# Kernel tuning notes

Hardware: AMD Instinct MI355X
Metric: run time of the kernel (lower is better)

The kernel has to match this reference:

```python
import jax, jax.numpy as jnp
import numpy as np

EPS = 1e-5
SLOPE = 0.01  # LeakyReLU default negative_slope
D_STATE = 16


def leaky(x):
    return jnp.where(x >= 0, x, SLOPE * x)


def instance_norm(x):
    # InstanceNorm3d(affine=False): normalize per (n, c) over spatial dims
    m = x.mean(axis=(2, 3, 4), keepdims=True)
    v = x.var(axis=(2, 3, 4), keepdims=True)
    return (x - m) * jax.lax.rsqrt(v + EPS)


def conv3d(x, w, b, groups=1, pad=0):
    y = jax.lax.conv_general_dilated(
        x, w, (1, 1, 1), [(pad, pad)] * 3,
        dimension_numbers=('NCDHW', 'OIDHW', 'NCDHW'),
        feature_group_count=groups)
    return y + b[None, :, None, None, None]


def conv_transpose2(x, w, b):
    # ConvTranspose3d(k=2, s=2): non-overlapping, so it is a pure einsum+interleave
    # x: [n,c,d,h,w], w: [c,o,2,2,2] (torch layout)
    y = jnp.einsum('ncdhw,coijk->nodihjwk', x, w)
    n, o, d, _, h, _, ww, _ = y.shape
    return y.reshape(n, o, 2 * d, 2 * h, 2 * ww) + b[None, :, None, None, None]


def selective_scan(u, dt, A, B, C, D):
    # u, dt: [b,l,d]; A: [d,n]; B, C: [b,l,n]; D: [d]
    dA = jnp.exp(dt[..., None] * A)                              # [b,l,d,n]
    dBu = dt[..., None] * B[:, :, None, :] * u[..., None]        # [b,l,d,n]

    def step(h, inp):
        dA_t, dBu_t, C_t = inp
        h = dA_t * h + dBu_t                                     # [b,d,n]
        y = jnp.einsum('bdn,bn->bd', h, C_t)
        return h, y

    h0 = jnp.zeros((u.shape[0],) + A.shape, u.dtype)
    _, ys = jax.lax.scan(
        step, h0,
        (dA.transpose(1, 0, 2, 3), dBu.transpose(1, 0, 2, 3), C.transpose(1, 0, 2)))
    return ys.transpose(1, 0, 2) + u * D                         # [b,l,d]


def mamba_block(x, in_proj_w, conv1d_w, conv1d_b, x_proj_w,
                dt_proj_w, dt_proj_b, A_log, D_param, out_proj_w):
    # x: [b,l,c]
    dt_rank = dt_proj_w.shape[1]
    xz = x @ in_proj_w.T                                         # [b,l,2*d_inner]
    xi, z = jnp.split(xz, 2, axis=-1)
    # causal depthwise conv1d over sequence (torch pads d_conv-1 both sides, keeps [:L])
    xi_c = xi.transpose(0, 2, 1)                                 # [b,d_inner,l]
    xi_c = jax.lax.conv_general_dilated(
        xi_c, conv1d_w, (1,), [(conv1d_w.shape[-1] - 1, 0)],
        dimension_numbers=('NCH', 'OIH', 'NCH'),
        feature_group_count=xi_c.shape[1])
    xi = jax.nn.silu(xi_c + conv1d_b[None, :, None]).transpose(0, 2, 1)  # [b,l,d_inner]
    x_dbl = xi @ x_proj_w.T
    dt, B, C = jnp.split(x_dbl, [dt_rank, dt_rank + D_STATE], axis=-1)
    dt = jax.nn.softplus(dt @ dt_proj_w.T + dt_proj_b)
    A = -jnp.exp(A_log)
    y = selective_scan(xi, dt, A, B, C, D_param)
    y = y * jax.nn.silu(z)
    return y @ out_proj_w.T


def layer_norm(x, w, b):
    m = x.mean(-1, keepdims=True)
    v = x.var(-1, keepdims=True)
    return (x - m) * jax.lax.rsqrt(v + EPS) * w + b


def up_forward(x1, x2, up_w, up_b, dc1_w, dc1_b, dc2_w, dc2_b, dc3_w, dc3_b,
               ln_w, ln_b, in_proj_w, conv1d_w, conv1d_b, x_proj_w,
               dt_proj_w, dt_proj_b, A_log, D_param, out_proj_w):
    x1 = conv_transpose2(x1, up_w, up_b)
    dZ = x2.shape[2] - x1.shape[2]
    dY = x2.shape[3] - x1.shape[3]
    dX = x2.shape[4] - x1.shape[4]
    x1 = jnp.pad(x1, ((0, 0), (0, 0),
                      (dZ // 2, dZ - dZ // 2),
                      (dY // 2, dY - dY // 2),
                      (dX // 2, dX - dX // 2)))
    x = jnp.concatenate([x2, x1], axis=1)
    # DoubleConv (residual=False since in_channels != out_channels)
    x = leaky(instance_norm(conv3d(x, dc1_w, dc1_b)))
    x = leaky(instance_norm(conv3d(x, dc2_w, dc2_b, groups=8, pad=1)))
    x = leaky(instance_norm(conv3d(x, dc3_w, dc3_b)))
    # MambaLayer over flattened spatial tokens
    b, c, d, h, w = x.shape
    t = x.transpose(0, 2, 3, 4, 1).reshape(b, d * h * w, c)
    t = layer_norm(t, ln_w, ln_b)
    t = mamba_block(t, in_proj_w, conv1d_w, conv1d_b, x_proj_w,
                    dt_proj_w, dt_proj_b, A_log, D_param, out_proj_w)
    return t.reshape(b, d, h, w, c).transpose(0, 4, 1, 2, 3)


def setup_inputs() -> dict:
    key = jax.random.key(0)
    ks = jax.random.split(key, 20)
    c_out = 32      # out_channels / d_model
    d_inner = 64    # expand * d_model
    dt_rank = 2     # ceil(32/16)
    s = 0.02
    return {
        'x1': jax.random.normal(ks[0], (2, 32, 8, 16, 16), jnp.float32),
        'x2': jax.random.normal(ks[1], (2, 32, 16, 32, 32), jnp.float32),
        'up_w': jax.random.normal(ks[2], (32, 32, 2, 2, 2), jnp.float32) * s,
        'up_b': jnp.zeros((32,), jnp.float32),
        'dc1_w': jax.random.normal(ks[3], (32, 64, 1, 1, 1), jnp.float32) * s,
        'dc1_b': jnp.zeros((32,), jnp.float32),
        'dc2_w': jax.random.normal(ks[4], (32, 4, 3, 3, 3), jnp.float32) * s,
        'dc2_b': jnp.zeros((32,), jnp.float32),
        'dc3_w': jax.random.normal(ks[5], (32, 32, 1, 1, 1), jnp.float32) * s,
        'dc3_b': jnp.zeros((32,), jnp.float32),
        'ln_w': jnp.ones((c_out,), jnp.float32),
        'ln_b': jnp.zeros((c_out,), jnp.float32),
        'in_proj_w': jax.random.normal(ks[6], (2 * d_inner, c_out), jnp.float32) * s,
        'conv1d_w': jax.random.normal(ks[7], (d_inner, 1, 4), jnp.float32) * s,
        'conv1d_b': jnp.zeros((d_inner,), jnp.float32),
        'x_proj_w': jax.random.normal(ks[8], (dt_rank + 2 * D_STATE, d_inner), jnp.float32) * s,
        'dt_proj_w': jax.random.normal(ks[9], (d_inner, dt_rank), jnp.float32) * s,
        'dt_proj_b': jnp.full((d_inner,), -4.0, jnp.float32),
        'A_log': jnp.log(jnp.tile(jnp.arange(1.0, D_STATE + 1.0, dtype=jnp.float32), (d_inner, 1))),
        'D_param': jnp.ones((d_inner,), jnp.float32),
        'out_proj_w': jax.random.normal(ks[10], (c_out, d_inner), jnp.float32) * s,
    }


def reference(x1, x2, up_w, up_b, dc1_w, dc1_b, dc2_w, dc2_b, dc3_w, dc3_b,
              ln_w, ln_b, in_proj_w, conv1d_w, conv1d_b, x_proj_w,
              dt_proj_w, dt_proj_b, A_log, D_param, out_proj_w):
    return up_forward(x1, x2, up_w, up_b, dc1_w, dc1_b, dc2_w, dc2_b, dc3_w, dc3_b,
                      ln_w, ln_b, in_proj_w, conv1d_w, conv1d_b, x_proj_w,
                      dt_proj_w, dt_proj_b, A_log, D_param, out_proj_w)
```

## Files before the change

kernel.cpp:

```cpp
#include <hip/hip_runtime.h>

#define TPB 256
#define S_TOT 16384
#define NCHUNK 256
#define EPS 1e-5f
#define SLOPE 0.01f

__device__ __forceinline__ float leakyf(float v){ return v > 0.f ? v : SLOPE * v; }
__device__ __forceinline__ float siluf(float v){ return v / (1.f + __expf(-v)); }

__global__ __launch_bounds__(TPB) void k_upc1(
    const float* __restrict__ x1, const float* __restrict__ x2,
    const float* __restrict__ upw, const float* __restrict__ upb,
    const float* __restrict__ w1, const float* __restrict__ b1,
    float* __restrict__ c1, float* st1p) {
  __shared__ float wq[8192];
  __shared__ float sup[64*33];
  __shared__ float red[4][8][2];
  int t = threadIdx.x, bid = blockIdx.x;
  int sb = bid & 255, n = bid >> 8;
  int p = t & 63, os = t >> 6;
  int s = sb*64 + p;
  for (int i = t; i < 8192; i += TPB) wq[i] = upw[i];
  __syncthreads();
  int z = s >> 10, y = (s >> 5) & 31, x = s & 31;
  int tap = ((z & 1)*2 + (y & 1))*2 + (x & 1);
  int xb = n*65536 + (z >> 1)*256 + (y >> 1)*16 + (x >> 1);
  float xv[32];
  #pragma unroll
  for (int c = 0; c < 32; c++) xv[c] = x1[xb + c*2048];
  float up[8];
  #pragma unroll
  for (int j = 0; j < 8; j++) up[j] = upb[os*8 + j];
  #pragma unroll
  for (int c = 0; c < 32; c++) {
    #pragma unroll
    for (int j = 0; j < 8; j++)
      up[j] += xv[c] * wq[c*256 + (os*8 + j)*8 + tap];
  }
  #pragma unroll
  for (int j = 0; j < 8; j++) sup[p*33 + os*8 + j] = up[j];
  __syncthreads();
  int c0 = os*8;
  float acc[8];
  #pragma unroll
  for (int j = 0; j < 8; j++) acc[j] = b1[c0 + j];
  const float* px2 = x2 + n*32*S_TOT + s;
  #pragma unroll
  for (int i = 0; i < 32; i++) {
    float v = px2[i*S_TOT];
    #pragma unroll
    for (int j = 0; j < 8; j++) acc[j] += v * w1[(c0 + j)*64 + i];
  }
  #pragma unroll
  for (int o = 0; o < 32; o++) {
    float v = sup[p*33 + o];
    #pragma unroll
    for (int j = 0; j < 8; j++) acc[j] += v * w1[(c0 + j)*64 + 32 + o];
  }
  #pragma unroll
  for (int j = 0; j < 8; j++)
    c1[(n*32 + c0 + j)*S_TOT + s] = acc[j];
  int wv = t >> 6;
  #pragma unroll
  for (int j = 0; j < 8; j++) {
    float sm = acc[j], sq = acc[j]*acc[j];
    #pragma unroll
    for (int o = 32; o > 0; o >>= 1) { sm += __shfl_down(sm, o); sq += __shfl_down(sq, o); }
    if ((t & 63) == 0) { red[wv][j][0] = sm; red[wv][j][1] = sq; }
  }
  __syncthreads();
  if (t < 64) {
    int w2 = t >> 4, j = (t >> 1) & 7, m = t & 1;
    st1p[((n*32 + w2*8 + j)*2 + m)*256 + sb] = red[w2][j][m];
  }
}

__global__ __launch_bounds__(TPB) void k_conv2(
    const float* __restrict__ c1, const float* __restrict__ w,
    const float* __restrict__ bias, const float* st1p,
    float* __restrict__ c2, float* st2p) {
  __shared__ float ws[432];
  __shared__ float smom[4][2];
  __shared__ float mrs[4][2];
  __shared__ float red[4][4][2];
  int bid = blockIdx.x, t = threadIdx.x;
  int sb = bid & 63, g = (bid >> 6) & 7, n = bid >> 9;
  int s = (sb << 8) + t;
  for (int i = t; i < 432; i += TPB) ws[i] = w[(g*4)*108 + i];
  {
    int pp = t >> 5, l = t & 31;
    if (pp < 8) {
      int j = pp & 3, m = pp >> 2;
      const float* sp = st1p + ((n*32 + g*4 + j)*2 + m)*256;
      float v = 0.f;
      #pragma unroll
      for (int k = 0; k < 8; k++) v += sp[l + 32*k];
      v += __shfl_down(v, 16); v += __shfl_down(v, 8); v += __shfl_down(v, 4);
      v += __shfl_down(v, 2);  v += __shfl_down(v, 1);
      if (l == 0) smom[j][m] = v;
    }
  }
  __syncthreads();
  if (t < 4) {
    float m = smom[t][0] * (1.f/S_TOT);
    mrs[t][0] = m; mrs[t][1] = rsqrtf(smom[t][1]*(1.f/S_TOT) - m*m + EPS);
  }
  __syncthreads();
  int z = s >> 10, y = (s >> 5) & 31, x = s & 31;
  float mx0 = (x > 0) ? 1.f : 0.f, mx2 = (x < 31) ? 1.f : 0.f;
  float acc[4];
  #pragma unroll
  for (int oc = 0; oc < 4; oc++) acc[oc] = bias[g*4 + oc];
  const float* pbase = c1 + (n*32 + g*4)*S_TOT;
  #pragma unroll
  for (int ic = 0; ic < 4; ic++) {
    const float* pc = pbase + ic*S_TOT;
    float m = mrs[ic][0], rs = mrs[ic][1];
    #pragma unroll
    for (int dz = 0; dz < 3; dz++) {
      int zz = z + dz - 1;
      int zc = zz < 0 ? 0 : (zz > 15 ? 15 : zz);
      float vz = (zz >= 0 && zz < 16) ? 1.f : 0.f;
      #pragma unroll
      for (int dy = 0; dy < 3; dy++) {
        int yy = y + dy - 1;
        int yc = yy < 0 ? 0 : (yy > 31 ? 31 : yy);
        float vzy = vz * ((yy >= 0 && yy < 32) ? 1.f : 0.f);
        const float* pr = pc + zc*1024 + yc*32 + x;
        float p0 = leakyf((pr[-1] - m)*rs) * (vzy*mx0);
        float p1 = leakyf((pr[ 0] - m)*rs) * vzy;
        float p2 = leakyf((pr[ 1] - m)*rs) * (vzy*mx2);
        int wb = ic*27 + dz*9 + dy*3;
        #pragma unroll
        for (int oc = 0; oc < 4; oc++) {
          const float* wo = &ws[oc*108 + wb];
          acc[oc] += p0*wo[0] + p1*wo[1] + p2*wo[2];
        }
      }
    }
  }
  float sm[4], sq[4];
  #pragma unroll
  for (int oc = 0; oc < 4; oc++) {
    c2[(n*32 + g*4 + oc)*S_TOT + s] = acc[oc];
    sm[oc] = acc[oc]; sq[oc] = acc[oc]*acc[oc];
  }
  #pragma unroll
  for (int o = 32; o > 0; o >>= 1) {
    #pragma unroll
    for (int oc = 0; oc < 4; oc++) {
      sm[oc] += __shfl_down(sm[oc], o);
      sq[oc] += __shfl_down(sq[oc], o);
    }
  }
  int lane = t & 63, wv = t >> 6;
  if (lane == 0) {
    #pragma unroll
    for (int oc = 0; oc < 4; oc++) { red[wv][oc][0] = sm[oc]; red[wv][oc][1] = sq[oc]; }
  }
  __syncthreads();
  if (t < 8) {
    int oc = t & 3, m = t >> 2;
    float a = red[0][oc][m] + red[1][oc][m] + red[2][oc][m] + red[3][oc][m];
    st2p[((n*32 + g*4 + oc)*2 + m)*64 + sb] = a;
  }
}

__global__ __launch_bounds__(TPB) void k_conv3(
    const float* __restrict__ c2, const float* __restrict__ w,
    const float* __restrict__ bias, const float* st2p,
    float* __restrict__ c3, float* st3p) {
  __shared__ float ws[256];
  __shared__ float ssum[32][2];
  __shared__ float mrs[32][2];
  __shared__ float red[4][8][2];
  int t = threadIdx.x;
  int idx = blockIdx.x * TPB + t;
  int s = idx & 16383;
  int n = (idx >> 14) & 1;
  int q = idx >> 15;
  int sb = blockIdx.x & 63;
  int c0 = q*8;
  if (t < 256) ws[t] = w[c0*32 + t];
  if (t < 64) {
    int c = t >> 1, m = t & 1;
    const float* sp = st2p + ((n*32 + c)*2 + m)*64;
    float v = 0.f;
    #pragma unroll
    for (int k = 0; k < 64; k++) v += sp[k];
    ssum[c][m] = v;
  }
  __syncthreads();
  if (t < 32) {
    float m = ssum[t][0] * (1.f/S_TOT);
    mrs[t][0] = m; mrs[t][1] = rsqrtf(ssum[t][1]*(1.f/S_TOT) - m*m + EPS);
  }
  __syncthreads();
  const float* pin = c2 + n*32*S_TOT + s;
  float acc[8];
  #pragma unroll
  for (int j = 0; j < 8; j++) acc[j] = bias[c0 + j];
  #pragma unroll
  for (int i = 0; i < 32; i++) {
    float v = leakyf((pin[i*S_TOT] - mrs[i][0]) * mrs[i][1]);
    #pragma unroll
    for (int j = 0; j < 8; j++) acc[j] += v * ws[j*32 + i];
  }
  #pragma unroll
  for (int j = 0; j < 8; j++)
    c3[(n*32 + c0 + j)*S_TOT + s] = acc[j];
  int wv = t >> 6;
  #pragma unroll
  for (int j = 0; j < 8; j++) {
    float sm = acc[j], sq = acc[j]*acc[j];
    #pragma unroll
    for (int o = 32; o > 0; o >>= 1) { sm += __shfl_down(sm, o); sq += __shfl_down(sq, o); }
    if ((t & 63) == 0) { red[wv][j][0] = sm; red[wv][j][1] = sq; }
  }
  __syncthreads();
  if (t < 16) {
    int j = t >> 1, m = t & 1;
    float a = red[0][j][m] + red[1][j][m] + red[2][j][m] + red[3][j][m];
    st3p[((n*32 + c0 + j)*2 + m)*64 + sb] = a;
  }
}

__global__ __launch_bounds__(TPB) void k_token(
    const float* __restrict__ c3, const float* st3p,
    const float* __restrict__ lnw, const float* __restrict__ lnb,
    const float* __restrict__ ipw, const float* __restrict__ c1w,
    const float* __restrict__ c1b, const float* __restrict__ xpw,
    const float* __restrict__ dtw, const float* __restrict__ dtbi,
    float* __restrict__ zb, float* __restrict__ u, float* __restrict__ dt,
    float* __restrict__ Bb, float* __restrict__ Cc) {
  __shared__ float W2T[4096];
  __shared__ float xpT[2176];
  __shared__ float tk[19*33];
  __shared__ float sxi[19*64];
  __shared__ float su2[16*65];
  __shared__ float xd[16*34];
  __shared__ float S1[128], S2[128];
  __shared__ float mv[19][2];
  __shared__ float mrs[32][2];
  __shared__ float ssum[32][2];
  int t = threadIdx.x, bid = blockIdx.x;
  int tok0 = bid * 16;
  int n = tok0 >> 14, s0 = tok0 & 16383;
  if (t < 64) {
    int c = t >> 1, m = t & 1;
    const float* sp = st3p + ((n*32 + c)*2 + m)*64;
    float v = 0.f;
    #pragma unroll
    for (int k = 0; k < 64; k++) v += sp[k];
    ssum[c][m] = v;
  }
  for (int i = t; i < 4096; i += TPB) {
    int f = i >> 5, c = i & 31;
    W2T[c*128 + f] = ipw[i] * lnw[c];
  }
  for (int i = t; i < 2176; i += TPB) {
    int f = i >> 6, dd = i & 63;
    xpT[dd*34 + f] = xpw[i];
  }
  __syncthreads();
  if (t < 32) {
    float m = ssum[t][0] * (1.f/S_TOT);
    mrs[t][0] = m; mrs[t][1] = rsqrtf(ssum[t][1]*(1.f/S_TOT) - m*m + EPS);
  }
  if (t < 128) {
    float a = 0.f, b2 = 0.f;
    #pragma unroll
    for (int c = 0; c < 32; c++) { a += W2T[c*128 + t]; b2 += ipw[t*32 + c]*lnb[c]; }
    S1[t] = a; S2[t] = b2;
  }
  __syncthreads();
  for (int i = t; i < 608; i += TPB) {
    int lt = i >> 5, c = i & 31;
    int sg = s0 - 3 + lt;
    int sgc = sg < 0 ? 0 : sg;
    float raw = c3[(n*32 + c)*S_TOT + sgc];
    tk[lt*33 + c] = leakyf((raw - mrs[c][0]) * mrs[c][1]);
  }
  __syncthreads();
  if (t < 19) {
    float mean = 0.f;
    #pragma unroll
    for (int c = 0; c < 32; c++) mean += tk[t*33 + c];
    mean *= (1.f/32.f);
    float var = 0.f;
    #pragma unroll
    for (int c = 0; c < 32; c++) { float d2 = tk[t*33 + c] - mean; var += d2*d2; }
    mv[t][0] = mean; mv[t][1] = rsqrtf(var*(1.f/32.f) + EPS);
  }
  __syncthreads();
  for (int i = t; i < 19*128; i += TPB) {
    int lt = i >> 7, f = i & 127;
    float acc = 0.f;
    #pragma unroll
    for (int c = 0; c < 32; c++) acc += W2T[c*128 + f] * tk[lt*33 + c];
    float r = mv[lt][1]*(acc - mv[lt][0]*S1[f]) + S2[f];
    int sg = s0 - 3 + lt;
    if (f < 64) {
      sxi[lt*64 + f] = (sg < 0) ? 0.f : r;
    } else if (lt >= 3) {
      zb[(tok0 + lt - 3)*64 + (f - 64)] = r;
    }
  }
  __syncthreads();
  int ch = t & 63;
  float cw0 = c1w[ch*4], cw1 = c1w[ch*4+1], cw2 = c1w[ch*4+2], cw3 = c1w[ch*4+3];
  float cb = c1b[ch];
  #pragma unroll
  for (int r = 0; r < 4; r++) {
    int lt = (t >> 6) + 4*r;
    float acc = cb + sxi[lt*64 + ch]*cw0 + sxi[(lt+1)*64 + ch]*cw1
                   + sxi[(lt+2)*64 + ch]*cw2 + sxi[(lt+3)*64 + ch]*cw3;
    float uv = siluf(acc);
    u[(tok0 + lt)*64 + ch] = uv;
    su2[lt*65 + ch] = uv;
  }
  __syncthreads();
  for (int i = t; i < 544; i += TPB) {
    int lt = i / 34, f = i - lt*34;
    float a = 0.f;
    #pragma unroll
    for (int dd = 0; dd < 64; dd++) a += xpT[dd*34 + f] * su2[lt*65 + dd];
    xd[lt*34 + f] = a;
  }
  __syncthreads();
  float dw0 = dtw[ch*2], dw1 = dtw[ch*2+1], db = dtbi[ch];
  #pragma unroll
  for (int r = 0; r < 4; r++) {
    int lt = (t >> 6) + 4*r;
    int token = tok0 + lt;
    float dv = xd[lt*34]*dw0 + xd[lt*34 + 1]*dw1 + db;
    dt[token*64 + ch] = fmaxf(dv, 0.f) + log1pf(__expf(-fabsf(dv)));
    if (ch < 16)      Bb[token*16 + ch]      = xd[lt*34 + 2 + ch];
    else if (ch < 32) Cc[token*16 + ch - 16] = xd[lt*34 + 2 + ch];
  }
}


__global__ __launch_bounds__(TPB) void k_scan1(
    const float* __restrict__ dt, const float* __restrict__ u,
    const float* __restrict__ Bb, const float* __restrict__ Alog,
    float* __restrict__ cA, float* __restrict__ cX) {
  __shared__ __align__(16) float sdt[1024], su[1024], sB[256];
  int bid = blockIdx.x, t = threadIdx.x;
  int chunk = bid & 255, b = bid >> 8;
  int q = t & 3, d = t >> 2;
  float Ar[4];
  #pragma unroll
  for (int j = 0; j < 4; j++) Ar[j] = -__expf(Alog[d*16 + 4*q + j]);
  float h[4] = {0.f,0.f,0.f,0.f};
  float sdts = 0.f;
  int tg0 = b*S_TOT + chunk*64;
  for (int tile = 0; tile < 4; tile++) {
    int base = tg0 + tile*16;
    for (int i = t; i < 1024; i += TPB) { sdt[i] = dt[base*64 + i]; su[i] = u[base*64 + i]; }
    sB[t] = Bb[base*16 + t];
    __syncthreads();
    #pragma unroll
    for (int tt = 0; tt < 16; tt++) {
      float dtv = sdt[tt*64 + d], uv = su[tt*64 + d];
      sdts += dtv;
      float du = dtv * uv;
      float4 Bq = *(const float4*)(sB + tt*16 + q*4);
      h[0] = __expf(Ar[0]*dtv)*h[0] + Bq.x*du;
      h[1] = __expf(Ar[1]*dtv)*h[1] + Bq.y*du;
      h[2] = __expf(Ar[2]*dtv)*h[2] + Bq.z*du;
      h[3] = __expf(Ar[3]*dtv)*h[3] + Bq.w*du;
    }
    __syncthreads();
  }
  #pragma unroll
  for (int j = 0; j < 4; j++) {
    int idx = (((b*64 + d)*16 + 4*q + j)*NCHUNK) + chunk;
    cA[idx] = __expf(Ar[j]*sdts);
    cX[idx] = h[j];
  }
}

__global__ __launch_bounds__(TPB) void k_scan2(
    const float* __restrict__ cA, float* __restrict__ cX) {
  int t = threadIdx.x;
  int w = blockIdx.x*4 + (t >> 6);
  int lane = t & 63;
  int b = w >> 10, d = (w >> 4) & 63, nn = w & 15;
  int base = ((b*64 + d)*16 + nn)*NCHUNK;
  float4 a = *(const float4*)(cA + base + lane*4);
  float4 x = *(const float4*)(cX + base + lane*4);
  float A = a.x*a.y*a.z*a.w;
  float X = ((x.x*a.y + x.y)*a.z + x.z)*a.w + x.w;
  #pragma unroll
  for (int off = 1; off < 64; off <<= 1) {
    float Ap = __shfl_up(A, off);
    float Xp = __shfl_up(X, off);
    if (lane >= off) { X = A*Xp + X; A = A*Ap; }
  }
  float Xe = __shfl_up(X, 1);
  if (lane == 0) Xe = 0.f;
  float r = Xe;
  float4 o;
  o.x = r; r = a.x*r + x.x;
  o.y = r; r = a.y*r + x.y;
  o.z = r; r = a.z*r + x.z;
  o.w = r;
  *(float4*)(cX + base + lane*4) = o;
}

__global__ __launch_bounds__(TPB) void k_scan3(
    const float* __restrict__ dt, const float* __restrict__ u,
    const float* __restrict__ Bb, const float* __restrict__ Cc,
    const float* __restrict__ Alog, const float* __restrict__ Dp,
    const float* __restrict__ zb, const float* __restrict__ cX,
    const float* __restrict__ opw, float* __restrict__ out) {
  __shared__ __align__(16) float sdt[1024], su[1024], sB[256], sC[256];
  __shared__ float gt[64*65];
  int bid = blockIdx.x, t = threadIdx.x;
  int chunk = bid & 255, b = bid >> 8;
  int q = t & 3, d = t >> 2;
  float Ar[4];
  #pragma unroll
  for (int j = 0; j < 4; j++) Ar[j] = -__expf(Alog[d*16 + 4*q + j]);
  float h[4];
  #pragma unroll
  for (int j = 0; j < 4; j++)
    h[j] = cX[(((b*64 + d)*16 + 4*q + j)*NCHUNK) + chunk];
  float Dv = Dp[d];
  int tg0 = b*S_TOT + chunk*64;
  for (int tile = 0; tile < 4; tile++) {
    int base = tg0 + tile*16;
    for (int i = t; i < 1024; i += TPB) {
      sdt[i] = dt[base*64 + i];
      su[i]  = u[base*64 + i];
      gt[(tile*16 + (i >> 6))*65 + (i & 63)] = zb[base*64 + i];
    }
    sB[t] = Bb[base*16 + t];
    sC[t] = Cc[base*16 + t];
    __syncthreads();
    #pragma unroll
    for (int tt = 0; tt < 16; tt++) {
      float dtv = sdt[tt*64 + d], uv = su[tt*64 + d];
      float du = dtv * uv;
      float4 Bq = *(const float4*)(sB + tt*16 + q*4);
      float4 Cq = *(const float4*)(sC + tt*16 + q*4);
      h[0] = __expf(Ar[0]*dtv)*h[0] + Bq.x*du;
      h[1] = __expf(Ar[1]*dtv)*h[1] + Bq.y*du;
      h[2] = __expf(Ar[2]*dtv)*h[2] + Bq.z*du;
      h[3] = __expf(Ar[3]*dtv)*h[3] + Bq.w*du;
      float yp = h[0]*Cq.x + h[1]*Cq.y + h[2]*Cq.z + h[3]*Cq.w;
      yp += __shfl_xor(yp, 1);
      yp += __shfl_xor(yp, 2);
      if (q == 0) {
        float zv = gt[(tile*16 + tt)*65 + d];
        gt[(tile*16 + tt)*65 + d] = (yp + uv*Dv) * siluf(zv);
      }
    }
    __syncthreads();
  }
  {
    int sl = t & 63, cb = t >> 6;
    float acc[8] = {0.f,0.f,0.f,0.f,0.f,0.f,0.f,0.f};
    const float* wp = opw + cb*8*64;
    #pragma unroll
    for (int dd = 0; dd < 64; dd++) {
      float v = gt[sl*65 + dd];
      #pragma unroll
      for (int j = 0; j < 8; j++) acc[j] += v * wp[j*64 + dd];
    }
    #pragma unroll
    for (int j = 0; j < 8; j++)
      out[(b*32 + cb*8 + j)*S_TOT + chunk*64 + sl] = acc[j];
  }
}

extern "C" void kernel_launch(void* const* d_in, const int* in_sizes, int n_in,
                              void* d_out, int out_size, void* d_ws, size_t ws_size,
                              hipStream_t stream) {
  const float* x1    = (const float*)d_in[0];
  const float* x2    = (const float*)d_in[1];
  const float* upw   = (const float*)d_in[2];
  const float* upb   = (const float*)d_in[3];
  const float* dc1w  = (const float*)d_in[4];
  const float* dc1b  = (const float*)d_in[5];
  const float* dc2w  = (const float*)d_in[6];
  const float* dc2b  = (const float*)d_in[7];
  const float* dc3w  = (const float*)d_in[8];
  const float* dc3b  = (const float*)d_in[9];
  const float* lnw   = (const float*)d_in[10];
  const float* lnb   = (const float*)d_in[11];
  const float* ipw   = (const float*)d_in[12];
  const float* c1w   = (const float*)d_in[13];
  const float* c1b   = (const float*)d_in[14];
  const float* xpw   = (const float*)d_in[15];
  const float* dtw   = (const float*)d_in[16];
  const float* dtbi  = (const float*)d_in[17];
  const float* Alog  = (const float*)d_in[18];
  const float* Dp    = (const float*)d_in[19];
  const float* opw   = (const float*)d_in[20];
  float* out = (float*)d_out;

  float* ws = (float*)d_ws;
  float* st1p  = ws + 0;
  float* st2p  = ws + 32768;
  float* st3p  = ws + 40960;
  float* c1    = ws + 49152;
  float* c2    = ws + 1097728;
  float* c3    = ws + 2146304;
  float* zb    = ws + 3194880;
  float* ub    = ws + 5292032;
  float* dtb   = ws + 7389184;
  float* Bb    = ws + 9486336;
  float* Cc    = ws + 10010624;
  float* cA    = ws + 10534912;
  float* cX    = ws + 11059200;

  k_upc1 <<<512,  TPB, 0, stream>>>(x1, x2, upw, upb, dc1w, dc1b, c1, st1p);
  k_conv2<<<1024, TPB, 0, stream>>>(c1, dc2w, dc2b, st1p, c2, st2p);
  k_conv3<<<512,  TPB, 0, stream>>>(c2, dc3w, dc3b, st2p, c3, st3p);
  k_token<<<2048, TPB, 0, stream>>>(c3, st3p, lnw, lnb, ipw, c1w, c1b, xpw,
                                    dtw, dtbi, zb, ub, dtb, Bb, Cc);
  k_scan1<<<512,  TPB, 0, stream>>>(dtb, ub, Bb, Alog, cA, cX);
  k_scan2<<<512,  TPB, 0, stream>>>(cA, cX);
  k_scan3<<<512,  TPB, 0, stream>>>(dtb, ub, Bb, Cc, Alog, Dp, zb, cX, opw, out);
}
```

Baseline: 249.0 us.

## Fuse chunk-local scan pass into token kernel with 64-token blocks

The token-projection kernel now handles 64 tokens per block instead of 16, and runs the first selective-scan pass (per-chunk decay product and local state) directly from shared memory. This removes one launch and the re-read of dt/u/B from global memory. It also cuts the conv halo overhead per token and keeps the in_proj weights in registers with float4 shared loads. In exchange there are 4x fewer blocks (512), a large shared footprint (~55KB) that lowers occupancy, and a serial 64-step scan inside the block.

```diff
diff --git a/kernel.cpp b/kernel.cpp
--- a/kernel.cpp
+++ b/kernel.cpp
@@ -232,153 +232,181 @@
     const float* __restrict__ ipw, const float* __restrict__ c1w,
     const float* __restrict__ c1b, const float* __restrict__ xpw,
     const float* __restrict__ dtw, const float* __restrict__ dtbi,
+    const float* __restrict__ Alog,
     float* __restrict__ zb, float* __restrict__ u, float* __restrict__ dt,
-    float* __restrict__ Bb, float* __restrict__ Cc) {
-  __shared__ float W2T[4096];
-  __shared__ float xpT[2176];
-  __shared__ float tk[19*33];
-  __shared__ float sxi[19*64];
-  __shared__ float su2[16*65];
-  __shared__ float xd[16*34];
-  __shared__ float S1[128], S2[128];
-  __shared__ float mv[19][2];
-  __shared__ float mrs[32][2];
-  __shared__ float ssum[32][2];
+    float* __restrict__ Bb, float* __restrict__ Cc,
+    float* __restrict__ cA, float* __restrict__ cX) {
+  __shared__ float smem[13700];
+  float* xpf  = smem;
+  float* sxi  = smem + 2448;
+  float* sdt2 = smem + 2448;
+  float* mrs  = smem + 6736;
+  float* ssum = smem + 6800;
+  float* lnwb = smem + 6864;
+  float* un   = smem + 6928;
+  float* Wraw = un;
+  float* tk   = un + 4224;
+  float* mv   = un + 6636;
+  float* su2  = un;
+  float* xd   = un + 4352;
+
   int t = threadIdx.x, bid = blockIdx.x;
-  int tok0 = bid * 16;
-  int n = tok0 >> 14, s0 = tok0 & 16383;
+  int tok0 = bid * 64;
+  int n = bid >> 8, chunk = bid & 255;
+  int s0 = tok0 & 16383;
+
   if (t < 64) {
     int c = t >> 1, m = t & 1;
     const float* sp = st3p + ((n*32 + c)*2 + m)*64;
     float v = 0.f;
     #pragma unroll
     for (int k = 0; k < 64; k++) v += sp[k];
-    ssum[c][m] = v;
+    ssum[c*2 + m] = v;
   }
   for (int i = t; i < 4096; i += TPB) {
     int f = i >> 5, c = i & 31;
-    W2T[c*128 + f] = ipw[i] * lnw[c];
+    Wraw[f*33 + c] = ipw[i];
   }
   for (int i = t; i < 2176; i += TPB) {
     int f = i >> 6, dd = i & 63;
-    xpT[dd*34 + f] = xpw[i];
-  }
+    xpf[f*68 + dd] = xpw[i];
+  }
+  for (int i = 2448 - 136 + t; i < 2448; i += TPB) xpf[i] = 0.f;
+  if (t < 32) { lnwb[t] = lnw[t]; lnwb[32 + t] = lnb[t]; }
   __syncthreads();
   if (t < 32) {
-    float m = ssum[t][0] * (1.f/S_TOT);
-    mrs[t][0] = m; mrs[t][1] = rsqrtf(ssum[t][1]*(1.f/S_TOT) - m*m + EPS);
-  }
-  if (t < 128) {
-    float a = 0.f, b2 = 0.f;
-    #pragma unroll
-    for (int c = 0; c < 32; c++) { a += W2T[c*128 + t]; b2 += ipw[t*32 + c]*lnb[c]; }
-    S1[t] = a; S2[t] = b2;
-  }
-  __syncthreads();
-  for (int i = t; i < 608; i += TPB) {
-    int lt = i >> 5, c = i & 31;
+    float m = ssum[t*2] * (1.f/S_TOT);
+    mrs[t*2] = m; mrs[t*2 + 1] = rsqrtf(ssum[t*2 + 1]*(1.f/S_TOT) - m*m + EPS);
+  }
+  int ft = t & 63;
+  int f0 = 2*ft, f1 = 2*ft + 1;
+  float wl0[32], wl1[32];
+  float S1a = 0.f, S2a = 0.f, S1b = 0.f, S2b = 0.f;
+  __syncthreads();
+  #pragma unroll
+  for (int c = 0; c < 32; c++) {
+    float wa = Wraw[f0*33 + c], wb = Wraw[f1*33 + c];
+    float lw = lnwb[c], lb = lnwb[32 + c];
+    wl0[c] = wa*lw; wl1[c] = wb*lw;
+    S1a += wl0[c]; S2a += wa*lb;
+    S1b += wl1[c]; S2b += wb*lb;
+  }
+  for (int i = t; i < 2144; i += TPB) {
+    int c = i / 67, lt = i - c*67;
     int sg = s0 - 3 + lt;
     int sgc = sg < 0 ? 0 : sg;
     float raw = c3[(n*32 + c)*S_TOT + sgc];
-    tk[lt*33 + c] = leakyf((raw - mrs[c][0]) * mrs[c][1]);
-  }
-  __syncthreads();
-  if (t < 19) {
+    tk[lt*36 + c] = leakyf((raw - mrs[c*2]) * mrs[c*2 + 1]);
+  }
+  __syncthreads();
+  if (t < 67) {
     float mean = 0.f;
     #pragma unroll
-    for (int c = 0; c < 32; c++) mean += tk[t*33 + c];
+    for (int c = 0; c < 32; c++) mean += tk[t*36 + c];
     mean *= (1.f/32.f);
     float var = 0.f;
     #pragma unroll
-    for (int c = 0; c < 32; c++) { float d2 = tk[t*33 + c] - mean; var += d2*d2; }
-    mv[t][0] = mean; mv[t][1] = rsqrtf(var*(1.f/32.f) + EPS);
-  }
-  __syncthreads();
-  for (int i = t; i < 19*128; i += TPB) {
-    int lt = i >> 7, f = i & 127;
-    float acc = 0.f;
-    #pragma unroll
-    for (int c = 0; c < 32; c++) acc += W2T[c*128 + f] * tk[lt*33 + c];
-    float r = mv[lt][1]*(acc - mv[lt][0]*S1[f]) + S2[f];
-    int sg = s0 - 3 + lt;
-    if (f < 64) {
-      sxi[lt*64 + f] = (sg < 0) ? 0.f : r;
-    } else if (lt >= 3) {
-      zb[(tok0 + lt - 3)*64 + (f - 64)] = r;
+    for (int c = 0; c < 32; c++) { float d2 = tk[t*36 + c] - mean; var += d2*d2; }
+    mv[t*2] = mean; mv[t*2 + 1] = rsqrtf(var*(1.f/32.f) + EPS);
+  }
+  __syncthreads();
+  {
+    int gq = t >> 6;
+    int lt0 = gq*17, ltE = lt0 + 17; if (ltE > 67) ltE = 67;
+    for (int lt = lt0; lt < ltE; lt++) {
+      float a0 = 0.f, a1 = 0.f;
+      #pragma unroll
+      for (int c4 = 0; c4 < 8; c4++) {
+        float4 tq = *(const float4*)(tk + lt*36 + 4*c4);
+        a0 += wl0[4*c4]*tq.x + wl0[4*c4+1]*tq.y + wl0[4*c4+2]*tq.z + wl0[4*c4+3]*tq.w;
+        a1 += wl1[4*c4]*tq.x + wl1[4*c4+1]*tq.y + wl1[4*c4+2]*tq.z + wl1[4*c4+3]*tq.w;
+      }
+      float mean = mv[lt*2], rst = mv[lt*2 + 1];
+      float r0 = rst*(a0 - mean*S1a) + S2a;
+      float r1 = rst*(a1 - mean*S1b) + S2b;
+      int sg = s0 - 3 + lt;
+      if (ft < 32) {
+        float2 v; v.x = (sg < 0) ? 0.f : r0; v.y = (sg < 0) ? 0.f : r1;
+        *(float2*)(sxi + lt*64 + 2*ft) = v;
+      } else if (lt >= 3) {
+        float2 v; v.x = r0; v.y = r1;
+        *(float2*)(zb + (tok0 + lt - 3)*64 + (2*ft - 64)) = v;
+      }
     }
   }
   __syncthreads();
   int ch = t & 63;
-  float cw0 = c1w[ch*4], cw1 = c1w[ch*4+1], cw2 = c1w[ch*4+2], cw3 = c1w[ch*4+3];
-  float cb = c1b[ch];
-  #pragma unroll
-  for (int r = 0; r < 4; r++) {
-    int lt = (t >> 6) + 4*r;
-    float acc = cb + sxi[lt*64 + ch]*cw0 + sxi[(lt+1)*64 + ch]*cw1
-                   + sxi[(lt+2)*64 + ch]*cw2 + sxi[(lt+3)*64 + ch]*cw3;
-    float uv = siluf(acc);
-    u[(tok0 + lt)*64 + ch] = uv;
-    su2[lt*65 + ch] = uv;
-  }
-  __syncthreads();
-  for (int i = t; i < 544; i += TPB) {
-    int lt = i / 34, f = i - lt*34;
-    float a = 0.f;
-    #pragma unroll
-    for (int dd = 0; dd < 64; dd++) a += xpT[dd*34 + f] * su2[lt*65 + dd];
-    xd[lt*34 + f] = a;
-  }
-  __syncthreads();
-  float dw0 = dtw[ch*2], dw1 = dtw[ch*2+1], db = dtbi[ch];
-  #pragma unroll
-  for (int r = 0; r < 4; r++) {
-    int lt = (t >> 6) + 4*r;
-    int token = tok0 + lt;
-    float dv = xd[lt*34]*dw0 + xd[lt*34 + 1]*dw1 + db;
-    dt[token*64 + ch] = fmaxf(dv, 0.f) + log1pf(__expf(-fabsf(dv)));
-    if (ch < 16)      Bb[token*16 + ch]      = xd[lt*34 + 2 + ch];
-    else if (ch < 32) Cc[token*16 + ch - 16] = xd[lt*34 + 2 + ch];
-  }
-}
-
-
-__global__ __launch_bounds__(TPB) void k_scan1(
-    const float* __restrict__ dt, const float* __restrict__ u,
-    const float* __restrict__ Bb, const float* __restrict__ Alog,
-    float* __restrict__ cA, float* __restrict__ cX) {
-  __shared__ __align__(16) float sdt[1024], su[1024], sB[256];
-  int bid = blockIdx.x, t = threadIdx.x;
-  int chunk = bid & 255, b = bid >> 8;
-  int q = t & 3, d = t >> 2;
-  float Ar[4];
-  #pragma unroll
-  for (int j = 0; j < 4; j++) Ar[j] = -__expf(Alog[d*16 + 4*q + j]);
-  float h[4] = {0.f,0.f,0.f,0.f};
-  float sdts = 0.f;
-  int tg0 = b*S_TOT + chunk*64;
-  for (int tile = 0; tile < 4; tile++) {
-    int base = tg0 + tile*16;
-    for (int i = t; i < 1024; i += TPB) { sdt[i] = dt[base*64 + i]; su[i] = u[base*64 + i]; }
-    sB[t] = Bb[base*16 + t];
-    __syncthreads();
-    #pragma unroll
-    for (int tt = 0; tt < 16; tt++) {
-      float dtv = sdt[tt*64 + d], uv = su[tt*64 + d];
-      sdts += dtv;
+  {
+    float cw0 = c1w[ch*4], cw1 = c1w[ch*4+1], cw2 = c1w[ch*4+2], cw3 = c1w[ch*4+3];
+    float cb = c1b[ch];
+    #pragma unroll
+    for (int r = 0; r < 16; r++) {
+      int lt = (t >> 6) + 4*r;
+      float acc = cb + sxi[lt*64 + ch]*cw0 + sxi[(lt+1)*64 + ch]*cw1
+                     + sxi[(lt+2)*64 + ch]*cw2 + sxi[(lt+3)*64 + ch]*cw3;
+      float uv = siluf(acc);
+      u[(tok0 + lt)*64 + ch] = uv;
+      su2[lt*68 + ch] = uv;
+    }
+  }
+  __syncthreads();
+  {
+    int qx = t & 3, ltx = t >> 2;
+    int fb = qx*9;
+    float axx[9];
+    #pragma unroll
+    for (int j = 0; j < 9; j++) axx[j] = 0.f;
+    #pragma unroll
+    for (int c4 = 0; c4 < 16; c4++) {
+      float4 uq = *(const float4*)(su2 + ltx*68 + 4*c4);
+      #pragma unroll
+      for (int j = 0; j < 9; j++) {
+        float4 xq = *(const float4*)(xpf + (fb + j)*68 + 4*c4);
+        axx[j] += uq.x*xq.x + uq.y*xq.y + uq.z*xq.z + uq.w*xq.w;
+      }
+    }
+    #pragma unroll
+    for (int j = 0; j < 9; j++)
+      if (fb + j < 34) xd[ltx*34 + fb + j] = axx[j];
+  }
+  __syncthreads();
+  {
+    float dw0 = dtw[ch*2], dw1 = dtw[ch*2+1], db = dtbi[ch];
+    #pragma unroll
+    for (int r = 0; r < 16; r++) {
+      int lt = (t >> 6) + 4*r;
+      int token = tok0 + lt;
+      float dv = xd[lt*34]*dw0 + xd[lt*34 + 1]*dw1 + db;
+      float sp = fmaxf(dv, 0.f) + log1pf(__expf(-fabsf(dv)));
+      dt[token*64 + ch] = sp;
+      sdt2[lt*64 + ch] = sp;
+      if (ch < 16)      Bb[token*16 + ch]      = xd[lt*34 + 2 + ch];
+      else if (ch < 32) Cc[token*16 + ch - 16] = xd[lt*34 + 2 + ch];
+    }
+  }
+  __syncthreads();
+  {
+    int q = t & 3, d = t >> 2;
+    float Ar[4];
+    #pragma unroll
+    for (int j = 0; j < 4; j++) Ar[j] = -__expf(Alog[d*16 + 4*q + j]);
+    float h0 = 0.f, h1 = 0.f, h2 = 0.f, h3 = 0.f, sd = 0.f;
+    for (int tt = 0; tt < 64; tt++) {
+      float dtv = sdt2[tt*64 + d], uv = su2[tt*68 + d];
+      sd += dtv;
       float du = dtv * uv;
-      float4 Bq = *(const float4*)(sB + tt*16 + q*4);
-      h[0] = __expf(Ar[0]*dtv)*h[0] + Bq.x*du;
-      h[1] = __expf(Ar[1]*dtv)*h[1] + Bq.y*du;
-      h[2] = __expf(Ar[2]*dtv)*h[2] + Bq.z*du;
-      h[3] = __expf(Ar[3]*dtv)*h[3] + Bq.w*du;
-    }
-    __syncthreads();
-  }
-  #pragma unroll
-  for (int j = 0; j < 4; j++) {
-    int idx = (((b*64 + d)*16 + 4*q + j)*NCHUNK) + chunk;
-    cA[idx] = __expf(Ar[j]*sdts);
-    cX[idx] = h[j];
+      const float* bp = xd + tt*34 + 2 + 4*q;
+      float B0 = bp[0], B1 = bp[1], B2 = bp[2], B3 = bp[3];
+      h0 = __expf(Ar[0]*dtv)*h0 + B0*du;
+      h1 = __expf(Ar[1]*dtv)*h1 + B1*du;
+      h2 = __expf(Ar[2]*dtv)*h2 + B2*du;
+      h3 = __expf(Ar[3]*dtv)*h3 + B3*du;
+    }
+    int base = (((n*64 + d)*16 + 4*q)*NCHUNK) + chunk;
+    cA[base]            = __expf(Ar[0]*sd); cX[base]            = h0;
+    cA[base + NCHUNK]   = __expf(Ar[1]*sd); cX[base + NCHUNK]   = h1;
+    cA[base + 2*NCHUNK] = __expf(Ar[2]*sd); cX[base + 2*NCHUNK] = h2;
+    cA[base + 3*NCHUNK] = __expf(Ar[3]*sd); cX[base + 3*NCHUNK] = h3;
   }
 }
 
@@ -520,9 +548,8 @@
   k_upc1 <<<512,  TPB, 0, stream>>>(x1, x2, upw, upb, dc1w, dc1b, c1, st1p);
   k_conv2<<<1024, TPB, 0, stream>>>(c1, dc2w, dc2b, st1p, c2, st2p);
   k_conv3<<<512,  TPB, 0, stream>>>(c2, dc3w, dc3b, st2p, c3, st3p);
-  k_token<<<2048, TPB, 0, stream>>>(c3, st3p, lnw, lnb, ipw, c1w, c1b, xpw,
-                                    dtw, dtbi, zb, ub, dtb, Bb, Cc);
-  k_scan1<<<512,  TPB, 0, stream>>>(dtb, ub, Bb, Alog, cA, cX);
+  k_token<<<512,  TPB, 0, stream>>>(c3, st3p, lnw, lnb, ipw, c1w, c1b, xpw,
+                                    dtw, dtbi, Alog, zb, ub, dtb, Bb, Cc, cA, cX);
   k_scan2<<<512,  TPB, 0, stream>>>(cA, cX);
   k_scan3<<<512,  TPB, 0, stream>>>(dtb, ub, Bb, Cc, Alog, Dp, zb, cX, opw, out);
 }
```

Result: slower. 268.8 us (+7.9%).
